# Performance work log

Hardware: AMD Instinct MI355X
Metric: run time of the kernel (lower is better)

## Reference

```python
import jax, jax.numpy as jnp
from jax import lax
import numpy as np

N, I, H, B, T = 16, 128, 128, 32, 512  # n lstms, input_size, hidden_size, batch, seq_len


def setup_inputs() -> dict:
    key = jax.random.key(0)
    k0, k1, k2, k3, k4 = jax.random.split(key, 5)
    s = 1.0 / np.sqrt(H)  # PyTorch LSTM init scale U(-1/sqrt(H), 1/sqrt(H)); normal*s is fine numerically
    x = jax.random.normal(k0, (B, T, N * I), dtype=jnp.float32)
    W_ih = jax.random.normal(k1, (N, 4 * H, I), dtype=jnp.float32) * s
    W_hh = jax.random.normal(k2, (N, 4 * H, H), dtype=jnp.float32) * s
    b_ih = jax.random.normal(k3, (N, 4 * H), dtype=jnp.float32) * s
    b_hh = jax.random.normal(k4, (N, 4 * H), dtype=jnp.float32) * s
    return {"x": x, "W_ih": W_ih, "W_hh": W_hh, "b_ih": b_ih, "b_hh": b_hh}


def reference(x, W_ih, W_hh, b_ih, b_hh):
    """WideLSTM fused forward: N independent single-layer unidirectional LSTMs,
    hx=None (zero initial state), batch_first output [B, T, N*H], (h_n, c_n) [1, B, N*H].
    PyTorch gate order: i, f, g, o."""
    Bx, Tx, _ = x.shape
    n = W_ih.shape[0]
    h = W_hh.shape[-1]
    xs = x.reshape(Bx, Tx, n, -1).transpose(1, 0, 2, 3)  # [T, B, N, I]
    # Precompute input contribution + biases for all timesteps at once (one big GEMM)
    x_proj = jnp.einsum('tbni,ngi->tbng', xs, W_ih) + (b_ih + b_hh)  # [T, B, N, 4H]

    def step(carry, xp):
        hprev, cprev = carry
        z = xp + jnp.einsum('bnh,ngh->bng', hprev, W_hh)  # [B, N, 4H]
        i_g, f_g, g_g, o_g = jnp.split(z, 4, axis=-1)
        i_g = jax.nn.sigmoid(i_g)
        f_g = jax.nn.sigmoid(f_g)
        g_g = jnp.tanh(g_g)
        o_g = jax.nn.sigmoid(o_g)
        c = f_g * cprev + i_g * g_g
        hnew = o_g * jnp.tanh(c)
        return (hnew, c), hnew

    h0 = jnp.zeros((Bx, n, h), dtype=x.dtype)
    c0 = jnp.zeros((Bx, n, h), dtype=x.dtype)
    (h_n, c_n), hs = lax.scan(step, (h0, c0), x_proj)
    output = hs.transpose(1, 0, 2, 3).reshape(Bx, Tx, n * h)  # [B, T, N*H]
    h_n = h_n.reshape(1, Bx, n * h)  # [num_layers*num_dir=1, B, N*H]
    c_n = c_n.reshape(1, Bx, n * h)
    return output, h_n, c_n
```

## Files before the change

kernel.cpp:

```cpp
#include <hip/hip_runtime.h>

#define N_LSTM 16
#define ISZ 128
#define HSZ 128
#define BSZ 32
#define TSZ 512
#define G4H 512
#define XROW (N_LSTM * ISZ)
#define OROW (N_LSTM * HSZ)

typedef __attribute__((ext_vector_type(8))) short s16x8;
typedef __attribute__((ext_vector_type(4))) float f32x4;

static __device__ __forceinline__ unsigned short f2bf(float f) {
    unsigned int u = __builtin_bit_cast(unsigned int, f);
    u += 0x7fffu + ((u >> 16) & 1u);
    return (unsigned short)(u >> 16);
}

static __device__ __forceinline__ float fast_sigmoid(float x) {
    float e = __expf(-x);
    return __builtin_amdgcn_rcpf(1.0f + e);
}

static __device__ __forceinline__ float fast_tanh(float x) {
    x = fminf(fmaxf(x, -20.0f), 20.0f);
    float e = __expf(-2.0f * x);
    return (1.0f - e) * __builtin_amdgcn_rcpf(1.0f + e);
}

__global__ __launch_bounds__(512, 2) void widelstm_fused(
    const float* __restrict__ x, const float* __restrict__ Wih,
    const float* __restrict__ Whh, const float* __restrict__ bih,
    const float* __restrict__ bhh, float* __restrict__ out)
{
    __shared__ __align__(16) unsigned short xbuf[2][16][136];
    __shared__ __align__(16) unsigned short hbuf[2][16][136];

    const int tid = threadIdx.x;
    const int wv  = tid >> 6;
    const int ln  = tid & 63;
    const int lm  = ln & 15;
    const int lq  = ln >> 4;
    const int n    = blockIdx.x >> 1;
    const int half = blockIdx.x & 1;
    const int b0   = half * 16;

    s16x8 wih[4][4], whh[4][4];
    float bias[4];
    #pragma unroll
    for (int g = 0; g < 4; ++g) {
        const int col = g * 128 + wv * 16 + lm;
        bias[g] = bih[n * G4H + col] + bhh[n * G4H + col];
        #pragma unroll
        for (int kt = 0; kt < 4; ++kt) {
            const float* pi = Wih + ((size_t)n * G4H + col) * ISZ + kt * 32 + lq * 8;
            const float* ph = Whh + ((size_t)n * G4H + col) * HSZ + kt * 32 + lq * 8;
            s16x8 a, b;
            #pragma unroll
            for (int j = 0; j < 8; ++j) {
                a[j] = (short)f2bf(pi[j]);
                b[j] = (short)f2bf(ph[j]);
            }
            wih[g][kt] = a;
            whh[g][kt] = b;
        }
    }

    for (int i = tid; i < 2 * 16 * 136; i += 512)
        ((unsigned short*)hbuf)[i] = 0;

    const int sr = tid >> 5;
    const int sc = (tid & 31) * 4;
    const float* xrow = x + (size_t)(b0 + sr) * TSZ * XROW + n * ISZ + sc;

    float4 xr = *(const float4*)(xrow);

    float cprev[4] = {0.f, 0.f, 0.f, 0.f};
    float hlast[4] = {0.f, 0.f, 0.f, 0.f};

    const int ocol = n * HSZ + wv * 16 + lm;

    #pragma unroll 1
    for (int t = 0; t < TSZ; ++t) {
        const int buf = t & 1;
        unsigned int lo = (unsigned int)f2bf(xr.x) | ((unsigned int)f2bf(xr.y) << 16);
        unsigned int hi = (unsigned int)f2bf(xr.z) | ((unsigned int)f2bf(xr.w) << 16);
        *(uint2*)&xbuf[buf][sr][sc] = make_uint2(lo, hi);
        __syncthreads();
        if (t + 1 < TSZ)
            xr = *(const float4*)(xrow + (size_t)(t + 1) * XROW);

        s16x8 ax[4], ah[4];
        #pragma unroll
        for (int kt = 0; kt < 4; ++kt) {
            ax[kt] = *(const s16x8*)&xbuf[buf][lm][kt * 32 + lq * 8];
            ah[kt] = *(const s16x8*)&hbuf[buf][lm][kt * 32 + lq * 8];
        }

        f32x4 acc[4];
        #pragma unroll
        for (int g = 0; g < 4; ++g)
            acc[g] = (f32x4){bias[g], bias[g], bias[g], bias[g]};
        #pragma unroll
        for (int kt = 0; kt < 4; ++kt) {
            #pragma unroll
            for (int g = 0; g < 4; ++g) {
                acc[g] = __builtin_amdgcn_mfma_f32_16x16x32_bf16(ax[kt], wih[g][kt], acc[g], 0, 0, 0);
                acc[g] = __builtin_amdgcn_mfma_f32_16x16x32_bf16(ah[kt], whh[g][kt], acc[g], 0, 0, 0);
            }
        }

        float* orow = out + (size_t)t * OROW + ocol;
        #pragma unroll
        for (int r = 0; r < 4; ++r) {
            float iv = fast_sigmoid(acc[0][r]);
            float fv = fast_sigmoid(acc[1][r]);
            float gv = fast_tanh(acc[2][r]);
            float ov = fast_sigmoid(acc[3][r]);
            float c  = fv * cprev[r] + iv * gv;
            cprev[r] = c;
            float hv = ov * fast_tanh(c);
            hlast[r] = hv;
            const int row = lq * 4 + r;
            orow[(size_t)(b0 + row) * TSZ * OROW] = hv;
            hbuf[buf ^ 1][row][wv * 16 + lm] = f2bf(hv);
        }
    }

    const size_t hn_off = (size_t)BSZ * TSZ * OROW;
    const size_t cn_off = hn_off + (size_t)BSZ * OROW;
    #pragma unroll
    for (int r = 0; r < 4; ++r) {
        const int row = lq * 4 + r;
        const size_t idx = (size_t)(b0 + row) * OROW + ocol;
        out[hn_off + idx] = hlast[r];
        out[cn_off + idx] = cprev[r];
    }
}

extern "C" void kernel_launch(void* const* d_in, const int* in_sizes, int n_in,
                              void* d_out, int out_size, void* d_ws, size_t ws_size,
                              hipStream_t stream) {
    const float* x   = (const float*)d_in[0];
    const float* Wih = (const float*)d_in[1];
    const float* Whh = (const float*)d_in[2];
    const float* bih = (const float*)d_in[3];
    const float* bhh = (const float*)d_in[4];
    float* out = (float*)d_out;
    widelstm_fused<<<dim3(32), dim3(512), 0, stream>>>(x, Wih, Whh, bih, bhh, out);
}
```

Before: 848.5 us.

## Precompute next-step input projection off the recurrent critical path

The input-projection MFMAs for step t+1 now run after the recurrent MFMAs for step t, and their results go into a separate accumulator that seeds the next step. This takes half the MFMA work off the serial dependency chain from h to gates. The loop is also unrolled by two with fixed buffer indices, and a custom barrier waits only on LDS counters. The cost is extra accumulator registers, and the hand-written barrier with scheduling fences may constrain compiler instruction reordering.

```diff
diff --git a/kernel.cpp b/kernel.cpp
--- a/kernel.cpp
+++ b/kernel.cpp
@@ -27,6 +27,13 @@
     x = fminf(fmaxf(x, -20.0f), 20.0f);
     float e = __expf(-2.0f * x);
     return (1.0f - e) * __builtin_amdgcn_rcpf(1.0f + e);
+}
+
+static __device__ __forceinline__ void barrier_lgkm() {
+    __builtin_amdgcn_sched_barrier(0);
+    asm volatile("s_waitcnt lgkmcnt(0)" ::: "memory");
+    __builtin_amdgcn_s_barrier();
+    __builtin_amdgcn_sched_barrier(0);
 }
 
 __global__ __launch_bounds__(512, 2) void widelstm_fused(
@@ -67,66 +74,101 @@
         }
     }
 
-    for (int i = tid; i < 2 * 16 * 136; i += 512)
-        ((unsigned short*)hbuf)[i] = 0;
+    for (int i = tid; i < 16 * 136; i += 512)
+        ((unsigned short*)hbuf[0])[i] = 0;
 
     const int sr = tid >> 5;
     const int sc = (tid & 31) * 4;
     const float* xrow = x + (size_t)(b0 + sr) * TSZ * XROW + n * ISZ + sc;
 
     float4 xr = *(const float4*)(xrow);
+    {
+        unsigned int lo = (unsigned int)f2bf(xr.x) | ((unsigned int)f2bf(xr.y) << 16);
+        unsigned int hi = (unsigned int)f2bf(xr.z) | ((unsigned int)f2bf(xr.w) << 16);
+        *(uint2*)&xbuf[0][sr][sc] = make_uint2(lo, hi);
+    }
+    barrier_lgkm();
+
+    f32x4 xacc[4];
+    #pragma unroll
+    for (int g = 0; g < 4; ++g)
+        xacc[g] = (f32x4){bias[g], bias[g], bias[g], bias[g]};
+    #pragma unroll
+    for (int kt = 0; kt < 4; ++kt) {
+        s16x8 axk = *(const s16x8*)&xbuf[0][lm][kt * 32 + lq * 8];
+        #pragma unroll
+        for (int g = 0; g < 4; ++g)
+            xacc[g] = __builtin_amdgcn_mfma_f32_16x16x32_bf16(axk, wih[g][kt], xacc[g], 0, 0, 0);
+    }
+
+    xr = *(const float4*)(xrow + (size_t)XROW);
 
     float cprev[4] = {0.f, 0.f, 0.f, 0.f};
     float hlast[4] = {0.f, 0.f, 0.f, 0.f};
-
     const int ocol = n * HSZ + wv * 16 + lm;
 
-    #pragma unroll 1
-    for (int t = 0; t < TSZ; ++t) {
-        const int buf = t & 1;
-        unsigned int lo = (unsigned int)f2bf(xr.x) | ((unsigned int)f2bf(xr.y) << 16);
-        unsigned int hi = (unsigned int)f2bf(xr.z) | ((unsigned int)f2bf(xr.w) << 16);
-        *(uint2*)&xbuf[buf][sr][sc] = make_uint2(lo, hi);
-        __syncthreads();
-        if (t + 1 < TSZ)
-            xr = *(const float4*)(xrow + (size_t)(t + 1) * XROW);
+#define LSTM_STEP(T_, CUR_, NXT_)                                                          \
+    {                                                                                      \
+        const int t_ = (T_);                                                               \
+        if (t_ + 1 < TSZ) {                                                                \
+            unsigned int lo = (unsigned int)f2bf(xr.x) | ((unsigned int)f2bf(xr.y) << 16); \
+            unsigned int hi = (unsigned int)f2bf(xr.z) | ((unsigned int)f2bf(xr.w) << 16); \
+            *(uint2*)&xbuf[NXT_][sr][sc] = make_uint2(lo, hi);                             \
+        }                                                                                  \
+        barrier_lgkm();                    \
+        s16x8 ah0 = *(const s16x8*)&hbuf[CUR_][lm][0 * 32 + lq * 8];                       \
+        s16x8 ah1 = *(const s16x8*)&hbuf[CUR_][lm][1 * 32 + lq * 8];                       \
+        s16x8 ah2 = *(const s16x8*)&hbuf[CUR_][lm][2 * 32 + lq * 8];                       \
+        s16x8 ah3 = *(const s16x8*)&hbuf[CUR_][lm][3 * 32 + lq * 8];                       \
+        if (t_ + 2 < TSZ)                                                                  \
+            xr = *(const float4*)(xrow + (size_t)(t_ + 2) * XROW);                         \
+        f32x4 hacc[4];                                                                     \
+        _Pragma("unroll")                                                                  \
+        for (int g = 0; g < 4; ++g)                                                        \
+            hacc[g] = __builtin_amdgcn_mfma_f32_16x16x32_bf16(ah0, whh[g][0], xacc[g], 0, 0, 0); \
+        _Pragma("unroll")                                                                  \
+        for (int g = 0; g < 4; ++g)                                                        \
+            hacc[g] = __builtin_amdgcn_mfma_f32_16x16x32_bf16(ah1, whh[g][1], hacc[g], 0, 0, 0); \
+        _Pragma("unroll")                                                                  \
+        for (int g = 0; g < 4; ++g)                                                        \
+            hacc[g] = __builtin_amdgcn_mfma_f32_16x16x32_bf16(ah2, whh[g][2], hacc[g], 0, 0, 0); \
+        _Pragma("unroll")                                                                  \
+        for (int g = 0; g < 4; ++g)                                                        \
+            hacc[g] = __builtin_amdgcn_mfma_f32_16x16x32_bf16(ah3, whh[g][3], hacc[g], 0, 0, 0); \
+        if (t_ + 1 < TSZ) {               \
+            _Pragma("unroll")                                                              \
+            for (int g = 0; g < 4; ++g)                                                    \
+                xacc[g] = (f32x4){bias[g], bias[g], bias[g], bias[g]};                     \
+            _Pragma("unroll")                                                              \
+            for (int kt = 0; kt < 4; ++kt) {                                               \
+                s16x8 axk = *(const s16x8*)&xbuf[NXT_][lm][kt * 32 + lq * 8];              \
+                _Pragma("unroll")                                                          \
+                for (int g = 0; g < 4; ++g)                                                \
+                    xacc[g] = __builtin_amdgcn_mfma_f32_16x16x32_bf16(axk, wih[g][kt], xacc[g], 0, 0, 0); \
+            }                                                                              \
+        }                                                                                  \
+        float* orow = out + (size_t)t_ * OROW + ocol;                                      \
+        _Pragma("unroll")                                                                  \
+        for (int r = 0; r < 4; ++r) {                                                      \
+            float iv = fast_sigmoid(hacc[0][r]);                                           \
+            float fv = fast_sigmoid(hacc[1][r]);                                           \
+            float gv = fast_tanh(hacc[2][r]);                                              \
+            float ov = fast_sigmoid(hacc[3][r]);                                           \
+            float c  = fv * cprev[r] + iv * gv;                                            \
+            cprev[r] = c;                                                                  \
+            float hv = ov * fast_tanh(c);                                                  \
+            hlast[r] = hv;                                                                 \
+            const int row = lq * 4 + r;                                                    \
+            orow[(size_t)(b0 + row) * TSZ * OROW] = hv;                                    \
+            hbuf[NXT_][row][wv * 16 + lm] = f2bf(hv);                                      \
+        }                                                                                  \
+    }
 
-        s16x8 ax[4], ah[4];
-        #pragma unroll
-        for (int kt = 0; kt < 4; ++kt) {
-            ax[kt] = *(const s16x8*)&xbuf[buf][lm][kt * 32 + lq * 8];
-            ah[kt] = *(const s16x8*)&hbuf[buf][lm][kt * 32 + lq * 8];
-        }
-
-        f32x4 acc[4];
-        #pragma unroll
-        for (int g = 0; g < 4; ++g)
-            acc[g] = (f32x4){bias[g], bias[g], bias[g], bias[g]};
-        #pragma unroll
-        for (int kt = 0; kt < 4; ++kt) {
-            #pragma unroll
-            for (int g = 0; g < 4; ++g) {
-                acc[g] = __builtin_amdgcn_mfma_f32_16x16x32_bf16(ax[kt], wih[g][kt], acc[g], 0, 0, 0);
-                acc[g] = __builtin_amdgcn_mfma_f32_16x16x32_bf16(ah[kt], whh[g][kt], acc[g], 0, 0, 0);
-            }
-        }
-
-        float* orow = out + (size_t)t * OROW + ocol;
-        #pragma unroll
-        for (int r = 0; r < 4; ++r) {
-            float iv = fast_sigmoid(acc[0][r]);
-            float fv = fast_sigmoid(acc[1][r]);
-            float gv = fast_tanh(acc[2][r]);
-            float ov = fast_sigmoid(acc[3][r]);
-            float c  = fv * cprev[r] + iv * gv;
-            cprev[r] = c;
-            float hv = ov * fast_tanh(c);
-            hlast[r] = hv;
-            const int row = lq * 4 + r;
-            orow[(size_t)(b0 + row) * TSZ * OROW] = hv;
-            hbuf[buf ^ 1][row][wv * 16 + lm] = f2bf(hv);
-        }
+    for (int t = 0; t < TSZ; t += 2) {
+        LSTM_STEP(t, 0, 1);
+        LSTM_STEP(t + 1, 1, 0);
     }
+#undef LSTM_STEP
 
     const size_t hn_off = (size_t)BSZ * TSZ * OROW;
     const size_t cn_off = hn_off + (size_t)BSZ * OROW;
```

Result: faster. 782.8 us (-7.7%).
